# Kernel optimization log

Measured on AMD Instinct MI355X. Metric: run time of the kernel, lower is better.

## Reference

```python
import jax, jax.numpy as jnp
import numpy as np

C = 1.0                 # ball curvature
SQRT_C = 1.0
EPS_PROJ = 4e-3         # geoopt float32 boundary eps for project()
MIN_NORM = 1e-15
ATANH_EPS = 1e-7        # clamp for arctanh domain (float32)


def _norm(x):
    return jnp.clip(jnp.linalg.norm(x, axis=-1, keepdims=True), MIN_NORM, None)


def _project(x):
    # clip points back inside the Poincare ball of radius (1-eps)/sqrt(c)
    n = _norm(x)
    maxn = (1.0 - EPS_PROJ) / SQRT_C
    return jnp.where(n > maxn, x / n * maxn, x)


def _artanh(z):
    return jnp.arctanh(jnp.clip(z, -1.0 + ATANH_EPS, 1.0 - ATANH_EPS))


def mobius_add(x, y):
    x2 = jnp.sum(x * x, axis=-1, keepdims=True)
    y2 = jnp.sum(y * y, axis=-1, keepdims=True)
    xy = jnp.sum(x * y, axis=-1, keepdims=True)
    num = (1.0 + 2.0 * C * xy + C * y2) * x + (1.0 - C * x2) * y
    den = 1.0 + 2.0 * C * xy + C * C * x2 * y2
    return num / jnp.clip(den, MIN_NORM, None)


def mobius_matvec(M, x):
    # x: [B, in], M: [out, in] -> [B, out]
    xn = _norm(x)
    mx = x @ M.T
    mxn = _norm(mx)
    res = jnp.tanh(mxn / xn * _artanh(SQRT_C * xn)) * (mx / (mxn * SQRT_C))
    is_zero = jnp.all(mx == 0, axis=-1, keepdims=True)
    return jnp.where(is_zero, jnp.zeros_like(res), res)


def logmap0(x):
    n = _norm(x)
    return x / (SQRT_C * n) * _artanh(SQRT_C * n)


def expmap0(u):
    n = _norm(u)
    return jnp.tanh(SQRT_C * n) * u / (SQRT_C * n)


def mobius_linear(x, W, b):
    h = _project(mobius_matvec(W, x))
    return _project(mobius_add(h, b))


def setup_inputs() -> dict:
    key = jax.random.key(0)
    ks = jax.random.split(key, 5)
    B, D_IN, D_H, D_OUT = 65536, 256, 512, 128
    x = 0.05 * jax.random.normal(ks[0], (B, D_IN), dtype=jnp.float32)  # inside ball
    W1 = jax.random.normal(ks[1], (D_H, D_IN), dtype=jnp.float32) / np.sqrt(D_IN)
    b1 = 0.01 * jax.random.normal(ks[2], (D_H,), dtype=jnp.float32)
    W2 = jax.random.normal(ks[3], (D_OUT, D_H), dtype=jnp.float32) / np.sqrt(D_H)
    b2 = 0.01 * jax.random.normal(ks[4], (D_OUT,), dtype=jnp.float32)
    return {"x": x, "W1": W1, "b1": b1, "W2": W2, "b2": b2}


def reference(x, W1, b1, W2, b2):
    # mobius_tanh: mobius_linear then mobius_fn_apply(tanh, .) = expmap0(tanh(logmap0(.)))
    h = mobius_linear(x, W1, b1)
    h = _project(expmap0(jnp.tanh(logmap0(h))))
    out = mobius_linear(h, W2, b2)
    return out
```

## Files before the change

kernel.cpp:

```cpp
#include <hip/hip_runtime.h>
#include <hip/hip_bf16.h>
#include <math.h>

#define MAXN 0.996f
#define MINN 1e-15f
#define ATEPS (1.0f - 1e-7f)

typedef unsigned short u16;
typedef __attribute__((ext_vector_type(8))) short bf16x8;
typedef __attribute__((ext_vector_type(16))) float fx16;

__device__ __forceinline__ u16 f2bf(float v) {
  union { __hip_bfloat16 b; u16 u; } cv; cv.b = __float2bfloat16(v); return cv.u;
}
__device__ __forceinline__ float bf2f(u16 u) {
  union { u16 u; __hip_bfloat16 b; } cv; cv.u = u; return __bfloat162float(cv.b);
}

__device__ __forceinline__ float ftanh(float x) {
  float ax = fabsf(x);
  float e = __expf(ax + ax);
  float r = 1.f - 2.f / (e + 1.f);
  return copysignf(r, x);
}
__device__ __forceinline__ float fatanh(float z) {
  return 0.5f * __logf((1.f + z) / (1.f - z));
}

__global__ void cvtW(const float* __restrict__ W1, const float* __restrict__ W2,
                     u16* __restrict__ w1h, u16* __restrict__ w1l,
                     u16* __restrict__ w2h, u16* __restrict__ w2l) {
  int c = blockIdx.x * 512 + threadIdx.x;
  const float* src;
  u16 *dh, *dl;
  if (c < 16384) {
    int lane = c & 63, blk = c >> 6;
    int kt = blk & 15, n32 = blk >> 4;
    int n = n32 * 32 + (lane & 31), k0 = kt * 16 + (lane >> 5) * 8;
    src = W1 + n * 256 + k0;
    dh = w1h + c * 8; dl = w1l + c * 8;
  } else {
    int c2 = c - 16384;
    int lane = c2 & 63, blk = c2 >> 6;
    int kt = blk & 31, n32 = blk >> 5;
    int n = n32 * 32 + (lane & 31), k0 = kt * 16 + (lane >> 5) * 8;
    src = W2 + n * 512 + k0;
    dh = w2h + c2 * 8; dl = w2l + c2 * 8;
  }
  union { u16 u[8]; bf16x8 v; } ph, pl;
#pragma unroll
  for (int e = 0; e < 8; e++) {
    float v = src[e];
    u16 h = f2bf(v);
    ph.u[e] = h; pl.u[e] = f2bf(v - bf2f(h));
  }
  *(bf16x8*)dh = ph.v;
  *(bf16x8*)dl = pl.v;
}


#define XLO   32768
#define B1S   65536
#define B2S   67584
#define XNL   68096
#define XN2L  68352
#define RED1  68608
#define RED2  70656
#define RED4  72704
#define BNO   74752
#define SYO   74816

__global__ __launch_bounds__(512, 4) void hyper(
    const float* __restrict__ X,
    const float* __restrict__ b1,
    const float* __restrict__ b2,
    const u16* __restrict__ w1h, const u16* __restrict__ w1l,
    const u16* __restrict__ w2h, const u16* __restrict__ w2l,
    float* __restrict__ out)
{
  __shared__ __align__(16) char smem[74824];
  float* b1s  = (float*)(smem + B1S);
  float* b2s  = (float*)(smem + B2S);
  float* xnl  = (float*)(smem + XNL);
  float* xn2l = (float*)(smem + XN2L);
  float* red1 = (float*)(smem + RED1);
  float* red2 = (float*)(smem + RED2);
  float* red4 = (float*)(smem + RED4);
  float* bno  = (float*)(smem + BNO);
  float* sy   = (float*)(smem + SYO);

  const int t = threadIdx.x;
  const int w = t >> 6, l = t & 63, l31 = l & 31, hi = l >> 5;
  const long rowBase = (long)blockIdx.x * 64;

  {
    const int m0 = t >> 3, sub = t & 7;
    const float* xg = X + (rowBase + m0) * 256;
    float ss = 0.f;
#pragma unroll
    for (int j = 0; j < 8; j++) {
      float4 v = *(const float4*)(xg + (sub + j * 8) * 4);
      ss += v.x*v.x + v.y*v.y + v.z*v.z + v.w*v.w;
      u16 h0 = f2bf(v.x), h1 = f2bf(v.y), h2 = f2bf(v.z), h3 = f2bf(v.w);
      short4 sh; sh.x = (short)h0; sh.y = (short)h1; sh.z = (short)h2; sh.w = (short)h3;
      short4 sl;
      sl.x = (short)f2bf(v.x - bf2f(h0)); sl.y = (short)f2bf(v.y - bf2f(h1));
      sl.z = (short)f2bf(v.z - bf2f(h2)); sl.w = (short)f2bf(v.w - bf2f(h3));
      int c4 = sub + j * 8;
      int g = c4 >> 1, p = c4 & 1;
      int byt = g * 1024 + ((m0 * 16) ^ ((g & 7) << 4)) + p * 8;
      *(short4*)(smem + byt) = sh;
      *(short4*)(smem + XLO + byt) = sl;
    }
    ss += __shfl_xor(ss, 1); ss += __shfl_xor(ss, 2); ss += __shfl_xor(ss, 4);
    if (sub == 0) xnl[m0] = sqrtf(ss);

    float bv = b1[t];
    b1s[t] = bv;
    float s1 = bv * bv;
    s1 += __shfl_xor(s1, 1); s1 += __shfl_xor(s1, 2); s1 += __shfl_xor(s1, 4);
    s1 += __shfl_xor(s1, 8); s1 += __shfl_xor(s1, 16); s1 += __shfl_xor(s1, 32);
    if (l == 0) bno[w] = s1;
    float cv2 = 0.f;
    if (t < 128) { cv2 = b2[t]; b2s[t] = cv2; }
    float s2 = cv2 * cv2;
    s2 += __shfl_xor(s2, 1); s2 += __shfl_xor(s2, 2); s2 += __shfl_xor(s2, 4);
    s2 += __shfl_xor(s2, 8); s2 += __shfl_xor(s2, 16); s2 += __shfl_xor(s2, 32);
    if (t < 128 && l == 0) bno[8 + w] = s2;
  }
  __syncthreads();
  if (t == 0) {
    float a = 0.f;
#pragma unroll
    for (int j = 0; j < 8; j++) a += bno[j];
    sy[0] = a;
  }
  if (t == 64) sy[1] = bno[8] + bno[9];

  fx16 acc[2][2];
#pragma unroll
  for (int a = 0; a < 2; a++)
#pragma unroll
    for (int b = 0; b < 2; b++)
#pragma unroll
      for (int r = 0; r < 16; r++) acc[a][b][r] = 0.f;

  const bf16x8* W1H = (const bf16x8*)w1h;
  const bf16x8* W1L = (const bf16x8*)w1l;
  const int w1b0 = ((w * 2 + 0) * 16) * 64 + hi * 32 + l31;
  const int w1b1 = ((w * 2 + 1) * 16) * 64 + hi * 32 + l31;
  const int xslot = l31 * 16;

#pragma unroll
  for (int kt = 0; kt < 16; kt++) {
    int g = kt * 2 + hi;
    int xb = g * 1024 + (xslot ^ ((g & 7) << 4));
    bf16x8 bh0 = *(const bf16x8*)(smem + xb);
    bf16x8 bh1 = *(const bf16x8*)(smem + xb + 512);
    bf16x8 bl0 = *(const bf16x8*)(smem + XLO + xb);
    bf16x8 bl1 = *(const bf16x8*)(smem + XLO + xb + 512);
    bf16x8 wh0 = W1H[w1b0 + kt * 64];
    bf16x8 wl0 = W1L[w1b0 + kt * 64];
    bf16x8 wh1 = W1H[w1b1 + kt * 64];
    bf16x8 wl1 = W1L[w1b1 + kt * 64];
    acc[0][0] = __builtin_amdgcn_mfma_f32_32x32x16_bf16(wh0, bh0, acc[0][0], 0, 0, 0);
    acc[0][1] = __builtin_amdgcn_mfma_f32_32x32x16_bf16(wh0, bh1, acc[0][1], 0, 0, 0);
    acc[0][0] = __builtin_amdgcn_mfma_f32_32x32x16_bf16(wh0, bl0, acc[0][0], 0, 0, 0);
    acc[0][1] = __builtin_amdgcn_mfma_f32_32x32x16_bf16(wh0, bl1, acc[0][1], 0, 0, 0);
    acc[0][0] = __builtin_amdgcn_mfma_f32_32x32x16_bf16(wl0, bh0, acc[0][0], 0, 0, 0);
    acc[0][1] = __builtin_amdgcn_mfma_f32_32x32x16_bf16(wl0, bh1, acc[0][1], 0, 0, 0);
    acc[1][0] = __builtin_amdgcn_mfma_f32_32x32x16_bf16(wh1, bh0, acc[1][0], 0, 0, 0);
    acc[1][1] = __builtin_amdgcn_mfma_f32_32x32x16_bf16(wh1, bh1, acc[1][1], 0, 0, 0);
    acc[1][0] = __builtin_amdgcn_mfma_f32_32x32x16_bf16(wh1, bl0, acc[1][0], 0, 0, 0);
    acc[1][1] = __builtin_amdgcn_mfma_f32_32x32x16_bf16(wh1, bl1, acc[1][1], 0, 0, 0);
    acc[1][0] = __builtin_amdgcn_mfma_f32_32x32x16_bf16(wl1, bh0, acc[1][0], 0, 0, 0);
    acc[1][1] = __builtin_amdgcn_mfma_f32_32x32x16_bf16(wl1, bh1, acc[1][1], 0, 0, 0);
  }

  float4 bf[2][4];
#pragma unroll
  for (int nt = 0; nt < 2; nt++)
#pragma unroll
    for (int qq = 0; qq < 4; qq++)
      bf[nt][qq] = *(const float4*)(b1s + w * 64 + nt * 32 + qq * 8 + hi * 4);
#pragma unroll
  for (int mt = 0; mt < 2; mt++) {
    float p1 = 0.f, p2 = 0.f;
#pragma unroll
    for (int nt = 0; nt < 2; nt++)
#pragma unroll
      for (int qq = 0; qq < 4; qq++) {
        float a0 = acc[nt][mt][qq*4+0], a1 = acc[nt][mt][qq*4+1];
        float a2 = acc[nt][mt][qq*4+2], a3 = acc[nt][mt][qq*4+3];
        p1 += a0*a0 + a1*a1 + a2*a2 + a3*a3;
        p2 += a0*bf[nt][qq].x + a1*bf[nt][qq].y + a2*bf[nt][qq].z + a3*bf[nt][qq].w;
      }
    p1 += __shfl_xor(p1, 32);
    p2 += __shfl_xor(p2, 32);
    if (l < 32) { red1[w * 64 + mt * 32 + l31] = p1; red2[w * 64 + mt * 32 + l31] = p2; }
  }
  __syncthreads();

#pragma unroll
  for (int mt = 0; mt < 2; mt++) {
    int m = mt * 32 + l31;
    float s2 = 0.f, xyr = 0.f;
#pragma unroll
    for (int j = 0; j < 8; j++) { s2 += red1[j * 64 + m]; xyr += red2[j * 64 + m]; }
    float xnv = fmaxf(xnl[m], MINN);
    float mxn = fmaxf(sqrtf(s2), MINN);
    float tv  = ftanh(mxn / xnv * fatanh(fminf(xnv, ATEPS)));
    float sc  = tv / mxn;
    float hn  = fmaxf(tv, MINN);
    if (hn > MAXN) { sc *= MAXN / hn; hn = MAXN; }
    float xy = sc * xyr;
    float y2 = sy[0];
    float x2 = hn * hn;
    float A  = 1.f + 2.f * xy + y2;
    float Bc = 1.f - x2;
    float den = fmaxf(1.f + 2.f * xy + x2 * y2, MINN);
    float Ai = A / den, Bi = Bc / den;
    float g2s = Ai*Ai*x2 + 2.f*Ai*Bi*xy + Bi*Bi*y2;
    float gn = fmaxf(sqrtf(g2s), MINN);
    float pf = (gn > MAXN) ? (MAXN / gn) : 1.f;
    float gnp = fminf(gn, MAXN);
    float csc = pf * fatanh(fminf(gnp, ATEPS)) / gnp;
    float Asc = Ai * sc;
    float p4 = 0.f;
#pragma unroll
    for (int nt = 0; nt < 2; nt++)
#pragma unroll
      for (int qq = 0; qq < 4; qq++) {
        float t0 = ftanh(csc * (Asc * acc[nt][mt][qq*4+0] + Bi * bf[nt][qq].x));
        float t1 = ftanh(csc * (Asc * acc[nt][mt][qq*4+1] + Bi * bf[nt][qq].y));
        float t2 = ftanh(csc * (Asc * acc[nt][mt][qq*4+2] + Bi * bf[nt][qq].z));
        float t3 = ftanh(csc * (Asc * acc[nt][mt][qq*4+3] + Bi * bf[nt][qq].w));
        acc[nt][mt][qq*4+0] = t0; acc[nt][mt][qq*4+1] = t1;
        acc[nt][mt][qq*4+2] = t2; acc[nt][mt][qq*4+3] = t3;
        p4 += t0*t0 + t1*t1 + t2*t2 + t3*t3;
      }
    p4 += __shfl_xor(p4, 32);
    if (l < 32) red4[w * 64 + m] = p4;
  }
  __syncthreads();

#pragma unroll
  for (int mt = 0; mt < 2; mt++) {
    int m = mt * 32 + l31;
    float t2 = 0.f;
#pragma unroll
    for (int j = 0; j < 8; j++) t2 += red4[j * 64 + m];
    float tn = fmaxf(sqrtf(t2), MINN);
    float tv2 = ftanh(tn);
    float sc4 = tv2 / tn;
    float on = tv2;
    if (on > MAXN) { sc4 *= MAXN / on; on = MAXN; }
    if (w == 0 && l < 32) xn2l[m] = fmaxf(on, MINN);
#pragma unroll
    for (int nt = 0; nt < 2; nt++)
#pragma unroll
      for (int qq = 0; qq < 4; qq++) {
        short4 sh;
        sh.x = (short)f2bf(acc[nt][mt][qq*4+0] * sc4);
        sh.y = (short)f2bf(acc[nt][mt][qq*4+1] * sc4);
        sh.z = (short)f2bf(acc[nt][mt][qq*4+2] * sc4);
        sh.w = (short)f2bf(acc[nt][mt][qq*4+3] * sc4);
        int g2i = w * 8 + nt * 4 + qq;
        int byt = g2i * 1024 + ((m * 16) ^ ((g2i & 7) << 4)) + hi * 8;
        *(short4*)(smem + byt) = sh;
      }
  }
  __syncthreads();

  const int tile = w & 3, mh = w >> 2;
  fx16 acc2;
#pragma unroll
  for (int r = 0; r < 16; r++) acc2[r] = 0.f;
  const bf16x8* W2H = (const bf16x8*)w2h;
  const bf16x8* W2L = (const bf16x8*)w2l;
  const int w2b = (tile * 32) * 64 + hi * 32 + l31;
  const int hslot = mh * 512 + l31 * 16;
#pragma unroll
  for (int kt = 0; kt < 32; kt++) {
    int g = kt * 2 + hi;
    int hb = g * 1024 + (hslot ^ ((g & 7) << 4));
    bf16x8 bh = *(const bf16x8*)(smem + hb);
    bf16x8 wh = W2H[w2b + kt * 64];
    bf16x8 wl = W2L[w2b + kt * 64];
    acc2 = __builtin_amdgcn_mfma_f32_32x32x16_bf16(wh, bh, acc2, 0, 0, 0);
    acc2 = __builtin_amdgcn_mfma_f32_32x32x16_bf16(wl, bh, acc2, 0, 0, 0);
  }

  const int m2 = mh * 32 + l31;
  float4 bf2[4];
#pragma unroll
  for (int qq = 0; qq < 4; qq++)
    bf2[qq] = *(const float4*)(b2s + tile * 32 + qq * 8 + hi * 4);
  {
    float p1 = 0.f, p2 = 0.f;
#pragma unroll
    for (int qq = 0; qq < 4; qq++) {
      float a0 = acc2[qq*4+0], a1 = acc2[qq*4+1], a2 = acc2[qq*4+2], a3 = acc2[qq*4+3];
      p1 += a0*a0 + a1*a1 + a2*a2 + a3*a3;
      p2 += a0*bf2[qq].x + a1*bf2[qq].y + a2*bf2[qq].z + a3*bf2[qq].w;
    }
    p1 += __shfl_xor(p1, 32);
    p2 += __shfl_xor(p2, 32);
    if (l < 32) { red1[tile * 64 + m2] = p1; red2[tile * 64 + m2] = p2; }
  }
  __syncthreads();
  {
    float s2 = red1[m2] + red1[64 + m2] + red1[128 + m2] + red1[192 + m2];
    float xyr = red2[m2] + red2[64 + m2] + red2[128 + m2] + red2[192 + m2];
    float xnv = xn2l[m2];
    float mxn = fmaxf(sqrtf(s2), MINN);
    float tv  = ftanh(mxn / xnv * fatanh(fminf(xnv, ATEPS)));
    float sc  = tv / mxn;
    float hn  = fmaxf(tv, MINN);
    if (hn > MAXN) { sc *= MAXN / hn; hn = MAXN; }
    float xy = sc * xyr;
    float y2 = sy[1];
    float x2 = hn * hn;
    float A  = 1.f + 2.f * xy + y2;
    float Bc = 1.f - x2;
    float den = fmaxf(1.f + 2.f * xy + x2 * y2, MINN);
    float Ai = A / den, Bi = Bc / den;
    float g2s = Ai*Ai*x2 + 2.f*Ai*Bi*xy + Bi*Bi*y2;
    float gn = fmaxf(sqrtf(g2s), MINN);
    float pf = (gn > MAXN) ? (MAXN / gn) : 1.f;
    float As = pf * Ai * sc, Bs = pf * Bi;
#pragma unroll
    for (int qq = 0; qq < 4; qq++) {
      float o0 = As * acc2[qq*4+0] + Bs * bf2[qq].x;
      float o1 = As * acc2[qq*4+1] + Bs * bf2[qq].y;
      float o2 = As * acc2[qq*4+2] + Bs * bf2[qq].z;
      float o3 = As * acc2[qq*4+3] + Bs * bf2[qq].w;
      int n0 = tile * 32 + qq * 8 + 4 * hi;
      int base = m2 * 512;
      *(float*)(smem + base + (((n0 + 0) * 4) ^ ((m2 & 7) << 4))) = o0;
      *(float*)(smem + base + (((n0 + 1) * 4) ^ ((m2 & 7) << 4))) = o1;
      *(float*)(smem + base + (((n0 + 2) * 4) ^ ((m2 & 7) << 4))) = o2;
      *(float*)(smem + base + (((n0 + 3) * 4) ^ ((m2 & 7) << 4))) = o3;
    }
  }
  __syncthreads();
  {
    const int m0 = t >> 3, c = (t & 7) * 16;
    float* og = out + (rowBase + m0) * 128 + c;
#pragma unroll
    for (int ch = 0; ch < 4; ch++) {
      float4 v = *(const float4*)(smem + m0 * 512 + (((c + ch * 4) * 4) ^ ((m0 & 7) << 4)));
      *(float4*)(og + ch * 4) = v;
    }
  }
}

extern "C" void kernel_launch(void* const* d_in, const int* in_sizes, int n_in,
                              void* d_out, int out_size, void* d_ws, size_t ws_size,
                              hipStream_t stream) {
  const float* x  = (const float*)d_in[0];
  const float* W1 = (const float*)d_in[1];
  const float* b1 = (const float*)d_in[2];
  const float* W2 = (const float*)d_in[3];
  const float* b2 = (const float*)d_in[4];
  float* o = (float*)d_out;

  const int B = in_sizes[0] / 256;

  u16* w1h = (u16*)d_ws;
  u16* w1l = w1h + 512 * 256;
  u16* w2h = w1l + 512 * 256;
  u16* w2l = w2h + 128 * 512;

  cvtW<<<48, 512, 0, stream>>>(W1, W2, w1h, w1l, w2h, w2l);
  hyper<<<B / 64, 512, 0, stream>>>(x, b1, b2, w1h, w1l, w2h, w2l, o);
}
```

Before: 193.8 us.

## Drop low-part split of X in first GEMM and reload bias from LDS

Stops splitting the input activations into bf16 high and low parts, so the first GEMM runs 8 instead of 12 MFMAs per k-step and no longer writes or reads the X-low tile in shared memory. The bias float4 values are now reloaded from LDS at each use rather than kept in registers, which lowers register pressure. The weight-conversion kernel is relaunched as 96 blocks of 256 threads, covering the same work. Accuracy drops because the low-order bits of X are no longer represented.

```diff
diff --git a/kernel.cpp b/kernel.cpp
--- a/kernel.cpp
+++ b/kernel.cpp
@@ -30,7 +30,7 @@
 __global__ void cvtW(const float* __restrict__ W1, const float* __restrict__ W2,
                      u16* __restrict__ w1h, u16* __restrict__ w1l,
                      u16* __restrict__ w2h, u16* __restrict__ w2l) {
-  int c = blockIdx.x * 512 + threadIdx.x;
+  int c = blockIdx.x * 256 + threadIdx.x;
   const float* src;
   u16 *dh, *dl;
   if (c < 16384) {
@@ -59,7 +59,6 @@
 }
 
 
-#define XLO   32768
 #define B1S   65536
 #define B2S   67584
 #define XNL   68096
@@ -101,16 +100,13 @@
     for (int j = 0; j < 8; j++) {
       float4 v = *(const float4*)(xg + (sub + j * 8) * 4);
       ss += v.x*v.x + v.y*v.y + v.z*v.z + v.w*v.w;
-      u16 h0 = f2bf(v.x), h1 = f2bf(v.y), h2 = f2bf(v.z), h3 = f2bf(v.w);
-      short4 sh; sh.x = (short)h0; sh.y = (short)h1; sh.z = (short)h2; sh.w = (short)h3;
-      short4 sl;
-      sl.x = (short)f2bf(v.x - bf2f(h0)); sl.y = (short)f2bf(v.y - bf2f(h1));
-      sl.z = (short)f2bf(v.z - bf2f(h2)); sl.w = (short)f2bf(v.w - bf2f(h3));
+      short4 sh;
+      sh.x = (short)f2bf(v.x); sh.y = (short)f2bf(v.y);
+      sh.z = (short)f2bf(v.z); sh.w = (short)f2bf(v.w);
       int c4 = sub + j * 8;
       int g = c4 >> 1, p = c4 & 1;
       int byt = g * 1024 + ((m0 * 16) ^ ((g & 7) << 4)) + p * 8;
       *(short4*)(smem + byt) = sh;
-      *(short4*)(smem + XLO + byt) = sl;
     }
     ss += __shfl_xor(ss, 1); ss += __shfl_xor(ss, 2); ss += __shfl_xor(ss, 4);
     if (sub == 0) xnl[m0] = sqrtf(ss);
@@ -157,32 +153,20 @@
     int xb = g * 1024 + (xslot ^ ((g & 7) << 4));
     bf16x8 bh0 = *(const bf16x8*)(smem + xb);
     bf16x8 bh1 = *(const bf16x8*)(smem + xb + 512);
-    bf16x8 bl0 = *(const bf16x8*)(smem + XLO + xb);
-    bf16x8 bl1 = *(const bf16x8*)(smem + XLO + xb + 512);
     bf16x8 wh0 = W1H[w1b0 + kt * 64];
     bf16x8 wl0 = W1L[w1b0 + kt * 64];
     bf16x8 wh1 = W1H[w1b1 + kt * 64];
     bf16x8 wl1 = W1L[w1b1 + kt * 64];
     acc[0][0] = __builtin_amdgcn_mfma_f32_32x32x16_bf16(wh0, bh0, acc[0][0], 0, 0, 0);
     acc[0][1] = __builtin_amdgcn_mfma_f32_32x32x16_bf16(wh0, bh1, acc[0][1], 0, 0, 0);
-    acc[0][0] = __builtin_amdgcn_mfma_f32_32x32x16_bf16(wh0, bl0, acc[0][0], 0, 0, 0);
-    acc[0][1] = __builtin_amdgcn_mfma_f32_32x32x16_bf16(wh0, bl1, acc[0][1], 0, 0, 0);
+    acc[1][0] = __builtin_amdgcn_mfma_f32_32x32x16_bf16(wh1, bh0, acc[1][0], 0, 0, 0);
+    acc[1][1] = __builtin_amdgcn_mfma_f32_32x32x16_bf16(wh1, bh1, acc[1][1], 0, 0, 0);
     acc[0][0] = __builtin_amdgcn_mfma_f32_32x32x16_bf16(wl0, bh0, acc[0][0], 0, 0, 0);
     acc[0][1] = __builtin_amdgcn_mfma_f32_32x32x16_bf16(wl0, bh1, acc[0][1], 0, 0, 0);
-    acc[1][0] = __builtin_amdgcn_mfma_f32_32x32x16_bf16(wh1, bh0, acc[1][0], 0, 0, 0);
-    acc[1][1] = __builtin_amdgcn_mfma_f32_32x32x16_bf16(wh1, bh1, acc[1][1], 0, 0, 0);
-    acc[1][0] = __builtin_amdgcn_mfma_f32_32x32x16_bf16(wh1, bl0, acc[1][0], 0, 0, 0);
-    acc[1][1] = __builtin_amdgcn_mfma_f32_32x32x16_bf16(wh1, bl1, acc[1][1], 0, 0, 0);
     acc[1][0] = __builtin_amdgcn_mfma_f32_32x32x16_bf16(wl1, bh0, acc[1][0], 0, 0, 0);
     acc[1][1] = __builtin_amdgcn_mfma_f32_32x32x16_bf16(wl1, bh1, acc[1][1], 0, 0, 0);
   }
 
-  float4 bf[2][4];
-#pragma unroll
-  for (int nt = 0; nt < 2; nt++)
-#pragma unroll
-    for (int qq = 0; qq < 4; qq++)
-      bf[nt][qq] = *(const float4*)(b1s + w * 64 + nt * 32 + qq * 8 + hi * 4);
 #pragma unroll
   for (int mt = 0; mt < 2; mt++) {
     float p1 = 0.f, p2 = 0.f;
@@ -190,10 +174,11 @@
     for (int nt = 0; nt < 2; nt++)
 #pragma unroll
       for (int qq = 0; qq < 4; qq++) {
+        float4 bv = *(const float4*)(b1s + w * 64 + nt * 32 + qq * 8 + hi * 4);
         float a0 = acc[nt][mt][qq*4+0], a1 = acc[nt][mt][qq*4+1];
         float a2 = acc[nt][mt][qq*4+2], a3 = acc[nt][mt][qq*4+3];
         p1 += a0*a0 + a1*a1 + a2*a2 + a3*a3;
-        p2 += a0*bf[nt][qq].x + a1*bf[nt][qq].y + a2*bf[nt][qq].z + a3*bf[nt][qq].w;
+        p2 += a0*bv.x + a1*bv.y + a2*bv.z + a3*bv.w;
       }
     p1 += __shfl_xor(p1, 32);
     p2 += __shfl_xor(p2, 32);
@@ -231,10 +216,11 @@
     for (int nt = 0; nt < 2; nt++)
 #pragma unroll
       for (int qq = 0; qq < 4; qq++) {
-        float t0 = ftanh(csc * (Asc * acc[nt][mt][qq*4+0] + Bi * bf[nt][qq].x));
-        float t1 = ftanh(csc * (Asc * acc[nt][mt][qq*4+1] + Bi * bf[nt][qq].y));
-        float t2 = ftanh(csc * (Asc * acc[nt][mt][qq*4+2] + Bi * bf[nt][qq].z));
-        float t3 = ftanh(csc * (Asc * acc[nt][mt][qq*4+3] + Bi * bf[nt][qq].w));
+        float4 bv = *(const float4*)(b1s + w * 64 + nt * 32 + qq * 8 + hi * 4);
+        float t0 = ftanh(csc * (Asc * acc[nt][mt][qq*4+0] + Bi * bv.x));
+        float t1 = ftanh(csc * (Asc * acc[nt][mt][qq*4+1] + Bi * bv.y));
+        float t2 = ftanh(csc * (Asc * acc[nt][mt][qq*4+2] + Bi * bv.z));
+        float t3 = ftanh(csc * (Asc * acc[nt][mt][qq*4+3] + Bi * bv.w));
         acc[nt][mt][qq*4+0] = t0; acc[nt][mt][qq*4+1] = t1;
         acc[nt][mt][qq*4+2] = t2; acc[nt][mt][qq*4+3] = t3;
         p4 += t0*t0 + t1*t1 + t2*t2 + t3*t3;
@@ -292,17 +278,14 @@
   }
 
   const int m2 = mh * 32 + l31;
-  float4 bf2[4];
-#pragma unroll
-  for (int qq = 0; qq < 4; qq++)
-    bf2[qq] = *(const float4*)(b2s + tile * 32 + qq * 8 + hi * 4);
   {
     float p1 = 0.f, p2 = 0.f;
 #pragma unroll
     for (int qq = 0; qq < 4; qq++) {
+      float4 bv = *(const float4*)(b2s + tile * 32 + qq * 8 + hi * 4);
       float a0 = acc2[qq*4+0], a1 = acc2[qq*4+1], a2 = acc2[qq*4+2], a3 = acc2[qq*4+3];
       p1 += a0*a0 + a1*a1 + a2*a2 + a3*a3;
-      p2 += a0*bf2[qq].x + a1*bf2[qq].y + a2*bf2[qq].z + a3*bf2[qq].w;
+      p2 += a0*bv.x + a1*bv.y + a2*bv.z + a3*bv.w;
     }
     p1 += __shfl_xor(p1, 32);
     p2 += __shfl_xor(p2, 32);
@@ -331,10 +314,11 @@
     float As = pf * Ai * sc, Bs = pf * Bi;
 #pragma unroll
     for (int qq = 0; qq < 4; qq++) {
-      float o0 = As * acc2[qq*4+0] + Bs * bf2[qq].x;
-      float o1 = As * acc2[qq*4+1] + Bs * bf2[qq].y;
-      float o2 = As * acc2[qq*4+2] + Bs * bf2[qq].z;
-      float o3 = As * acc2[qq*4+3] + Bs * bf2[qq].w;
+      float4 bv = *(const float4*)(b2s + tile * 32 + qq * 8 + hi * 4);
+      float o0 = As * acc2[qq*4+0] + Bs * bv.x;
+      float o1 = As * acc2[qq*4+1] + Bs * bv.y;
+      float o2 = As * acc2[qq*4+2] + Bs * bv.z;
+      float o3 = As * acc2[qq*4+3] + Bs * bv.w;
       int n0 = tile * 32 + qq * 8 + 4 * hi;
       int base = m2 * 512;
       *(float*)(smem + base + (((n0 + 0) * 4) ^ ((m2 & 7) << 4))) = o0;
@@ -372,6 +356,6 @@
   u16* w2h = w1l + 512 * 256;
   u16* w2l = w2h + 128 * 512;
 
-  cvtW<<<48, 512, 0, stream>>>(W1, W2, w1h, w1l, w2h, w2l);
+  cvtW<<<96, 256, 0, stream>>>(W1, W2, w1h, w1l, w2h, w2l);
   hyper<<<B / 64, 512, 0, stream>>>(x, b1, b2, w1h, w1l, w2h, w2l, o);
 }
```

Measured after the change: 171.4 us. 1.13x faster.
